# Kernel optimization log

Hardware: AMD Instinct MI355X
Metric: run time of the kernel (lower is better)

## Reference

```python
import jax, jax.numpy as jnp
import numpy as np

NUM_BUCKETS = 32
MAX_DISTANCE = 128
N_HEADS = 16
D_KV = 64


def relative_position_bucket(rel, num_buckets=NUM_BUCKETS, max_distance=MAX_DISTANCE):
    # bidirectional (encoder) bucketing, matches the torch reference
    nb = num_buckets // 2
    ret = (rel > 0).astype(jnp.int32) * nb
    rp = jnp.abs(rel)
    max_exact = nb // 2
    is_small = rp < max_exact
    # guard log(0); masked out by is_small anyway
    large = max_exact + (
        jnp.log(jnp.maximum(rp, 1).astype(jnp.float32) / max_exact)
        / np.log(max_distance / max_exact)
        * (nb - max_exact)
    ).astype(jnp.int32)
    large = jnp.minimum(large, nb - 1)
    return ret + jnp.where(is_small, rp, large)


def compute_bias(rel_bias_table, q_len, k_len):
    q_pos = jnp.arange(q_len)[:, None]
    k_pos = jnp.arange(k_len)[None, :]
    buckets = relative_position_bucket(k_pos - q_pos)  # [S, K]
    bias = rel_bias_table[buckets]                      # [S, K, H]
    return jnp.transpose(bias, (2, 0, 1))[None]         # [1, H, S, K]


def setup_inputs() -> dict:
    key = jax.random.key(0)
    ks = jax.random.split(key, 6)
    d_model, inner = 1024, N_HEADS * D_KV
    scale = 1.0 / np.sqrt(d_model)
    return {
        "hidden_states": jax.random.normal(ks[0], (4, 2048, d_model), jnp.float32),
        "Wq": jax.random.normal(ks[1], (d_model, inner), jnp.float32) * scale,
        "Wk": jax.random.normal(ks[2], (d_model, inner), jnp.float32) * scale,
        "Wv": jax.random.normal(ks[3], (d_model, inner), jnp.float32) * scale,
        "Wo": jax.random.normal(ks[4], (inner, d_model), jnp.float32) * scale,
        "rel_bias_table": jax.random.normal(ks[5], (NUM_BUCKETS, N_HEADS), jnp.float32),
    }


def reference(hidden_states, Wq, Wk, Wv, Wo, rel_bias_table):
    B, S, _ = hidden_states.shape
    K_len = S  # self-attention (key_value_states is None)
    q = (hidden_states @ Wq).reshape(B, S, N_HEADS, D_KV)
    k = (hidden_states @ Wk).reshape(B, K_len, N_HEADS, D_KV)
    v = (hidden_states @ Wv).reshape(B, K_len, N_HEADS, D_KV)
    # NOTE: T5 attention has no 1/sqrt(d_kv) scaling
    scores = jnp.einsum("bshd,bkhd->bhsk", q, k)
    pos_bias = compute_bias(rel_bias_table, S, K_len)
    attn = jax.nn.softmax(scores + pos_bias, axis=-1)
    out = jnp.einsum("bhsk,bkhd->bshd", attn, v).reshape(B, S, N_HEADS * D_KV)
    out = out @ Wo
    return (out, pos_bias)
```

## Files before the change

### kernel.cpp

```cpp
#include <hip/hip_runtime.h>
#include <cstdint>
#include <cstddef>

typedef unsigned short u16;
typedef unsigned int u32;
typedef __attribute__((ext_vector_type(8))) short bf16x8;
typedef __attribute__((ext_vector_type(4))) float f32x4;
typedef __attribute__((ext_vector_type(16))) float f32x16;
typedef __attribute__((ext_vector_type(2))) unsigned int u32x2;

#define MFMA(a, b, c)   __builtin_amdgcn_mfma_f32_16x16x32_bf16((a), (b), (c), 0, 0, 0)
#define MFMA32(a, b, c) __builtin_amdgcn_mfma_f32_32x32x16_bf16((a), (b), (c), 0, 0, 0)

typedef const __attribute__((address_space(1))) void gv1_t;
typedef __attribute__((address_space(3))) void lv3_t;
#define GLOAD_LDS16(g, l) __builtin_amdgcn_global_load_lds((gv1_t*)(g), (lv3_t*)(l), 16, 0, 0)

#define BATCH 4
#define SEQ 2048
#define DMODEL 1024
#define NHEAD 16
#define MROWS (BATCH * SEQ)
#define QKVN (3 * DMODEL)

#define LOG2E 1.44269504088896340736f

__device__ __forceinline__ u16 f2bf(float f) {
  u32 x = __builtin_bit_cast(u32, f);
  x += 0x7fffu + ((x >> 16) & 1u);
  return (u16)(x >> 16);
}

__device__ __forceinline__ u32 pkbf(float a, float b) {
  return (u32)f2bf(a) | ((u32)f2bf(b) << 16);
}

__device__ __forceinline__ u32x2 plswap(u32 a, u32 b) {
  return __builtin_amdgcn_permlane32_swap(a, b, false, false);
}

extern "C" __device__ float __ocml_exp2_f32(float);
__device__ __forceinline__ float exp2fast(float x) {
#if __has_builtin(__builtin_amdgcn_exp2f)
  return __builtin_amdgcn_exp2f(x);
#else
  return __ocml_exp2_f32(x);
#endif
}

__global__ __launch_bounds__(256) void convert_h(const float* __restrict__ H,
                                                 u16* __restrict__ Hb) {
  size_t i = (size_t)blockIdx.x * 1024 + threadIdx.x * 4;
  float4 v = *(const float4*)&H[i];
  uint2 o;
  o.x = pkbf(v.x, v.y);
  o.y = pkbf(v.z, v.w);
  *(uint2*)&Hb[i] = o;
}

__global__ void transpose_w(const float* __restrict__ Wq, const float* __restrict__ Wk,
                            const float* __restrict__ Wv, const float* __restrict__ Wo,
                            u16* __restrict__ Wt) {
  __shared__ u16 Ts[32][33];
  const float* W = (blockIdx.z == 0) ? Wq : (blockIdx.z == 1) ? Wk
                   : (blockIdx.z == 2) ? Wv : Wo;
  const float s = (blockIdx.z == 0) ? LOG2E : 1.0f;
  int x = threadIdx.x, y0 = threadIdx.y;
  int r0 = blockIdx.y * 32, c0 = blockIdx.x * 32;
  for (int yy = y0; yy < 32; yy += 8)
    Ts[yy][x] = f2bf(W[(size_t)(r0 + yy) * 1024 + c0 + x] * s);
  __syncthreads();
  for (int yy = y0; yy < 32; yy += 8)
    Wt[(size_t)(blockIdx.z * 1024 + c0 + yy) * 1024 + r0 + x] = Ts[x][yy];
}

__device__ __forceinline__ int rel_bucket(int rel) {
  int ret = (rel > 0) ? 16 : 0;
  int rp = (rel < 0) ? -rel : rel;
  if (rp < 8) return ret + rp;
  int i = 0;
  i += (rp >= 12); i += (rp >= 16); i += (rp >= 23); i += (rp >= 32);
  i += (rp >= 46); i += (rp >= 64); i += (rp >= 91);
  return ret + 8 + i;
}

__global__ __launch_bounds__(256) void build_bias_rel(const float* __restrict__ tbl,
                                                      float* __restrict__ brel,
                                                      float* __restrict__ brel2) {
  int h = blockIdx.x;
  for (int rix = threadIdx.x; rix < 4095; rix += 256) {
    float v = tbl[rel_bucket(rix - 2047) * NHEAD + h];
    brel[h * 4096 + rix] = v;
    brel2[h * 4096 + rix] = v * LOG2E;
  }
}

__global__ __launch_bounds__(256) void gemm_bf16k(const u16* __restrict__ A,
                                                  const u16* __restrict__ Bt,
                                                  u16* __restrict__ Cb, float* __restrict__ Cf,
                                                  int M, int N, int K) {
  __shared__ u16 As[128 * 32];
  __shared__ u16 Bs[128 * 32];
  const int t = threadIdx.x;
  const int w = t >> 6, lane = t & 63, quad = lane >> 4, l15 = lane & 15;
  const int wr = w >> 1, wc = w & 1;

  const int nwg = gridDim.x * gridDim.y;
  const int orig = blockIdx.y * gridDim.x + blockIdx.x;
  const int wg = (orig & 7) * (nwg >> 3) + (orig >> 3);
  const int bx = wg % gridDim.x, by = wg / gridDim.x;
  const int row0 = by * 128, col0 = bx * 128;

  f32x4 acc[4][4];
  #pragma unroll
  for (int i = 0; i < 4; ++i)
    #pragma unroll
    for (int j = 0; j < 4; ++j) acc[i][j] = (f32x4){0.f, 0.f, 0.f, 0.f};

  const int srow = lane >> 2, scol = (lane & 3) * 8;

  for (int k0 = 0; k0 < K; k0 += 32) {
    #pragma unroll
    for (int p = 0; p < 2; ++p) {
      const int rb = w * 32 + p * 16;
      GLOAD_LDS16(&A[(size_t)(row0 + rb + srow) * K + k0 + scol], &As[rb * 32]);
      GLOAD_LDS16(&Bt[(size_t)(col0 + rb + srow) * K + k0 + scol], &Bs[rb * 32]);
    }
    __syncthreads();
    bf16x8 af[4], bfr[4];
    #pragma unroll
    for (int i = 0; i < 4; ++i)
      af[i] = *(const bf16x8*)&As[(wr * 64 + i * 16 + l15) * 32 + quad * 8];
    #pragma unroll
    for (int j = 0; j < 4; ++j)
      bfr[j] = *(const bf16x8*)&Bs[(wc * 64 + j * 16 + l15) * 32 + quad * 8];
    #pragma unroll
    for (int i = 0; i < 4; ++i)
      #pragma unroll
      for (int j = 0; j < 4; ++j)
        acc[i][j] = MFMA(af[i], bfr[j], acc[i][j]);
    __syncthreads();
  }
  #pragma unroll
  for (int i = 0; i < 4; ++i) {
    #pragma unroll
    for (int j = 0; j < 4; ++j) {
      int col = col0 + wc * 64 + j * 16 + l15;
      #pragma unroll
      for (int r = 0; r < 4; ++r) {
        int row = row0 + wr * 64 + i * 16 + quad * 4 + r;
        if (Cb) Cb[(size_t)row * N + col] = f2bf(acc[i][j][r]);
        else    Cf[(size_t)row * N + col] = acc[i][j][r];
      }
    }
  }
}

__global__ __launch_bounds__(256) void transpose_v(const u16* __restrict__ QKV,
                                                   u16* __restrict__ Vt) {
  __shared__ u16 Ts[64 * 72];
  int st = blockIdx.x, bh = blockIdx.y;
  int b = bh >> 4, h = bh & 15;
  int t = threadIdx.x;
  #pragma unroll
  for (int p = 0; p < 2; ++p) {
    int c = t * 2 + p, r = c >> 3, cc = (c & 7) * 8;
    *(uint4*)&Ts[r * 72 + cc] =
        *(const uint4*)&QKV[(size_t)(b * SEQ + st * 64 + r) * QKVN + 2 * DMODEL + h * 64 + cc];
  }
  __syncthreads();
  #pragma unroll
  for (int p = 0; p < 2; ++p) {
    int c = t * 2 + p, d = c >> 3, s8 = (c & 7) * 8;
    union { u16 u[8]; uint4 v; } tmp;
    #pragma unroll
    for (int jj = 0; jj < 8; ++jj) tmp.u[jj] = Ts[(s8 + jj) * 72 + d];
    *(uint4*)&Vt[((size_t)(bh * 64 + d)) * SEQ + st * 64 + s8] = tmp.v;
  }
}

__global__ __launch_bounds__(256) void attn_fused(const u16* __restrict__ QKV,
                                                  const u16* __restrict__ Vt,
                                                  const float* __restrict__ brel,
                                                  const float* __restrict__ brel2,
                                                  u16* __restrict__ Aout,
                                                  float* __restrict__ pb) {
  __shared__ u16 Ks[2][64 * 72];
  __shared__ u16 Vs[2][64 * 72];
  const int orig = blockIdx.y * gridDim.x + blockIdx.x;
  const int wg = (orig & 7) * 128 + (orig >> 3);
  const int qt = wg & 15, bh = wg >> 4;
  const int b = bh >> 4, h = bh & 15;
  const int t = threadIdx.x;
  const int w = t >> 6, lane = t & 63, l31 = lane & 31, h5 = lane >> 5;
  const int qb = qt * 128;
  const int qw0 = qb + w * 32;
  const int qr = qw0 + l31;

  const float cpos = brel2[h * 4096 + 4040];
  const float cneg = brel2[h * 4096 + 54];
  const float cpu  = brel[h * 4096 + 4040];
  const float cnu  = brel[h * 4096 + 54];

  const u16* qptr = QKV + (size_t)(b * SEQ + qr) * QKVN + h * 64 + h5 * 8;
  bf16x8 qf[4];
  #pragma unroll
  for (int ks = 0; ks < 4; ++ks) qf[ks] = *(const bf16x8*)(qptr + ks * 16);

  float lsum = 0.f;
  f32x16 oacc[2];
  #pragma unroll
  for (int m = 0; m < 2; ++m)
    #pragma unroll
    for (int i = 0; i < 16; ++i) oacc[m][i] = 0.f;

  const int c0 = t * 2, c1 = c0 + 1;
  const int r0s = c0 >> 3, cc0 = (c0 & 7) * 8;
  const int r1s = c1 >> 3, cc1 = (c1 & 7) * 8;
  const size_t krow = (size_t)(b * SEQ) * QKVN + DMODEL + h * 64;
  const size_t vtrow = (size_t)bh * 64;
  const float* brow = brel2 + h * 4096 + 2047;

  uint4 ka0 = *(const uint4*)&QKV[krow + (size_t)r0s * QKVN + cc0];
  uint4 ka1 = *(const uint4*)&QKV[krow + (size_t)r1s * QKVN + cc1];
  uint4 va0 = *(const uint4*)&Vt[(vtrow + r0s) * SEQ + cc0];
  uint4 va1 = *(const uint4*)&Vt[(vtrow + r1s) * SEQ + cc1];
  *(uint4*)&Ks[0][r0s * 72 + cc0] = ka0;
  *(uint4*)&Ks[0][r1s * 72 + cc1] = ka1;
  *(uint4*)&Vs[0][r0s * 72 + cc0] = va0;
  *(uint4*)&Vs[0][r1s * 72 + cc1] = va1;
  __syncthreads();

  #pragma unroll 2
  for (int ti = 0; ti < SEQ / 64; ++ti) {
    const int kb = ti * 64;
    const int cur = ti & 1;
    const u16* Kc = Ks[cur];
    const u16* Vc = Vs[cur];

    if (ti + 1 < SEQ / 64) {
      ka0 = *(const uint4*)&QKV[krow + (size_t)(kb + 64 + r0s) * QKVN + cc0];
      ka1 = *(const uint4*)&QKV[krow + (size_t)(kb + 64 + r1s) * QKVN + cc1];
      va0 = *(const uint4*)&Vt[(vtrow + r0s) * SEQ + kb + 64 + cc0];
      va1 = *(const uint4*)&Vt[(vtrow + r1s) * SEQ + kb + 64 + cc1];
    }

    f32x16 sc[2];
    __builtin_amdgcn_s_setprio(1);
    #pragma unroll
    for (int m = 0; m < 2; ++m) {
      #pragma unroll
      for (int i = 0; i < 16; ++i) sc[m][i] = 0.f;
      #pragma unroll
      for (int ks = 0; ks < 4; ++ks) {
        bf16x8 kf = *(const bf16x8*)&Kc[(m * 32 + l31) * 72 + ks * 16 + h5 * 8];
        sc[m] = MFMA32(kf, qf[ks], sc[m]);
      }
    }
    __builtin_amdgcn_s_setprio(0);

    if ((ti & 3) == b) {
      const int pr = qb + (t >> 1);
      const int pc = kb + (t & 1) * 32;
      float* po = pb + ((size_t)(h * SEQ + pr)) * SEQ + pc;
      const int lo = pc - pr;
      if (lo >= 91 || lo + 31 <= -91) {
        const float c = (lo >= 91) ? cpu : cnu;
        const float4 vv = {c, c, c, c};
        #pragma unroll
        for (int i = 0; i < 8; ++i) *(float4*)&po[i * 4] = vv;
      } else {
        const float* bb = brel + h * 4096 + 2047 - pr + pc;
        #pragma unroll
        for (int i = 0; i < 8; ++i) {
          float4 vv;
          vv.x = bb[i * 4]; vv.y = bb[i * 4 + 1];
          vv.z = bb[i * 4 + 2]; vv.w = bb[i * 4 + 3];
          *(float4*)&po[i * 4] = vv;
        }
      }
    }

    bf16x8 bp[4];
    #pragma unroll
    for (int m = 0; m < 2; ++m) {
      const int kb32 = kb + 32 * m;
      if (kb32 >= qw0 + 122) {
        #pragma unroll
        for (int i = 0; i < 16; ++i) sc[m][i] += cpos;
      } else if (kb32 <= qw0 - 122) {
        #pragma unroll
        for (int i = 0; i < 16; ++i) sc[m][i] += cneg;
      } else {
        const float* bb = brow + kb32 + 4 * h5 - qr;
        #pragma unroll
        for (int i = 0; i < 16; ++i) sc[m][i] += bb[(i & 3) + 8 * (i >> 2)];
      }
      u32 w0[4], w1[4];
      #pragma unroll
      for (int tt = 0; tt < 4; ++tt) {
        float p0 = exp2fast(sc[m][4 * tt + 0]);
        float p1 = exp2fast(sc[m][4 * tt + 1]);
        float p2 = exp2fast(sc[m][4 * tt + 2]);
        float p3 = exp2fast(sc[m][4 * tt + 3]);
        lsum += (p0 + p1) + (p2 + p3);
        w0[tt] = pkbf(p0, p1);
        w1[tt] = pkbf(p2, p3);
      }
      u32x2 r0 = plswap(w0[0], w0[1]);
      u32x2 r1 = plswap(w1[0], w1[1]);
      u32x2 r2 = plswap(w0[2], w0[3]);
      u32x2 r3 = plswap(w1[2], w1[3]);
      union { u32 u[4]; bf16x8 v; } q0, q1;
      q0.u[0] = r0.x; q0.u[1] = r1.x; q0.u[2] = r0.y; q0.u[3] = r1.y;
      q1.u[0] = r2.x; q1.u[1] = r3.x; q1.u[2] = r2.y; q1.u[3] = r3.y;
      bp[2 * m]     = q0.v;
      bp[2 * m + 1] = q1.v;
    }

    __builtin_amdgcn_s_setprio(1);
    #pragma unroll
    for (int m2 = 0; m2 < 2; ++m2)
      #pragma unroll
      for (int ks = 0; ks < 4; ++ks) {
        bf16x8 vf = *(const bf16x8*)&Vc[(m2 * 32 + l31) * 72 + ks * 16 + h5 * 8];
        oacc[m2] = MFMA32(vf, bp[ks], oacc[m2]);
      }
    __builtin_amdgcn_s_setprio(0);

    if (ti + 1 < SEQ / 64) {
      u16* Kn = Ks[cur ^ 1];
      u16* Vn = Vs[cur ^ 1];
      *(uint4*)&Kn[r0s * 72 + cc0] = ka0;
      *(uint4*)&Kn[r1s * 72 + cc1] = ka1;
      *(uint4*)&Vn[r0s * 72 + cc0] = va0;
      *(uint4*)&Vn[r1s * 72 + cc1] = va1;
    }
    __syncthreads();
  }

  lsum += __shfl_xor(lsum, 32);
  const float inv = 1.0f / lsum;
  const size_t rowb = (size_t)(b * SEQ + qr) * DMODEL + h * 64;
  #pragma unroll
  for (int m2 = 0; m2 < 2; ++m2)
    #pragma unroll
    for (int tt = 0; tt < 4; ++tt) {
      uint2 o;
      o.x = pkbf(oacc[m2][4 * tt + 0] * inv, oacc[m2][4 * tt + 1] * inv);
      o.y = pkbf(oacc[m2][4 * tt + 2] * inv, oacc[m2][4 * tt + 3] * inv);
      *(uint2*)&Aout[rowb + 32 * m2 + 8 * tt + 4 * h5] = o;
    }
}

extern "C" void kernel_launch(void* const* d_in, const int* in_sizes, int n_in,
                              void* d_out, int out_size, void* d_ws, size_t ws_size,
                              hipStream_t stream) {
  (void)in_sizes; (void)n_in; (void)out_size; (void)ws_size;
  const float* H   = (const float*)d_in[0];
  const float* Wq  = (const float*)d_in[1];
  const float* Wk  = (const float*)d_in[2];
  const float* Wv  = (const float*)d_in[3];
  const float* Wo  = (const float*)d_in[4];
  const float* tbl = (const float*)d_in[5];

  float* out = (float*)d_out;
  float* pos_bias = out + (size_t)MROWS * DMODEL;

  char* ws = (char*)d_ws;
  u16* Hb     = (u16*)(ws);
  u16* Wt     = (u16*)(ws + 16777216);
  u16* QKV    = (u16*)(ws + 25165824);
  u16* Vt     = (u16*)(ws + 75497472);
  float* brel  = (float*)(ws + 92274688);
  float* brel2 = (float*)(ws + 92536832);

  convert_h<<<8192, 256, 0, stream>>>(H, Hb);
  transpose_w<<<dim3(32, 32, 4), dim3(32, 8), 0, stream>>>(Wq, Wk, Wv, Wo, Wt);
  build_bias_rel<<<16, 256, 0, stream>>>(tbl, brel, brel2);

  gemm_bf16k<<<dim3(QKVN / 128, MROWS / 128), 256, 0, stream>>>(
      Hb, Wt, QKV, nullptr, MROWS, QKVN, DMODEL);
  transpose_v<<<dim3(32, 64), 256, 0, stream>>>(QKV, Vt);
  attn_fused<<<dim3(16, 64), 256, 0, stream>>>(QKV, Vt, brel, brel2,
                                               Hb , pos_bias);
  gemm_bf16k<<<dim3(DMODEL / 128, MROWS / 128), 256, 0, stream>>>(
      Hb, Wt + (size_t)QKVN * DMODEL, nullptr, out, MROWS, DMODEL, DMODEL);
}
```

Before: 571.8 us.

## Fuse V transpose into QKV GEMM epilogue and software-pipeline PV MFMA

```diff
diff --git a/kernel.cpp b/kernel.cpp
--- a/kernel.cpp
+++ b/kernel.cpp
@@ -98,6 +98,7 @@
 __global__ __launch_bounds__(256) void gemm_bf16k(const u16* __restrict__ A,
                                                   const u16* __restrict__ Bt,
                                                   u16* __restrict__ Cb, float* __restrict__ Cf,
+                                                  u16* __restrict__ Vt,
                                                   int M, int N, int K) {
   __shared__ u16 As[128 * 32];
   __shared__ u16 Bs[128 * 32];
@@ -145,37 +146,25 @@
   for (int i = 0; i < 4; ++i) {
     #pragma unroll
     for (int j = 0; j < 4; ++j) {
-      int col = col0 + wc * 64 + j * 16 + l15;
-      #pragma unroll
-      for (int r = 0; r < 4; ++r) {
-        int row = row0 + wr * 64 + i * 16 + quad * 4 + r;
-        if (Cb) Cb[(size_t)row * N + col] = f2bf(acc[i][j][r]);
-        else    Cf[(size_t)row * N + col] = acc[i][j][r];
-      }
-    }
-  }
-}
-
-__global__ __launch_bounds__(256) void transpose_v(const u16* __restrict__ QKV,
-                                                   u16* __restrict__ Vt) {
-  __shared__ u16 Ts[64 * 72];
-  int st = blockIdx.x, bh = blockIdx.y;
-  int b = bh >> 4, h = bh & 15;
-  int t = threadIdx.x;
-  #pragma unroll
-  for (int p = 0; p < 2; ++p) {
-    int c = t * 2 + p, r = c >> 3, cc = (c & 7) * 8;
-    *(uint4*)&Ts[r * 72 + cc] =
-        *(const uint4*)&QKV[(size_t)(b * SEQ + st * 64 + r) * QKVN + 2 * DMODEL + h * 64 + cc];
-  }
-  __syncthreads();
-  #pragma unroll
-  for (int p = 0; p < 2; ++p) {
-    int c = t * 2 + p, d = c >> 3, s8 = (c & 7) * 8;
-    union { u16 u[8]; uint4 v; } tmp;
-    #pragma unroll
-    for (int jj = 0; jj < 8; ++jj) tmp.u[jj] = Ts[(s8 + jj) * 72 + d];
-    *(uint4*)&Vt[((size_t)(bh * 64 + d)) * SEQ + st * 64 + s8] = tmp.v;
+      const int col = col0 + wc * 64 + j * 16 + l15;
+      const int srow0 = row0 + wr * 64 + i * 16 + quad * 4;
+      if (Cf) {
+        #pragma unroll
+        for (int r = 0; r < 4; ++r)
+          Cf[(size_t)(srow0 + r) * N + col] = acc[i][j][r];
+      } else if (!Vt || col < 2 * DMODEL) {
+        #pragma unroll
+        for (int r = 0; r < 4; ++r)
+          Cb[(size_t)(srow0 + r) * N + col] = f2bf(acc[i][j][r]);
+      } else {
+        const int c2 = col - 2 * DMODEL, hh = c2 >> 6, dd = c2 & 63;
+        const int bb = srow0 >> 11, ss = srow0 & (SEQ - 1);
+        uint2 o;
+        o.x = pkbf(acc[i][j][0], acc[i][j][1]);
+        o.y = pkbf(acc[i][j][2], acc[i][j][3]);
+        *(uint2*)&Vt[((size_t)(bb * 16 + hh) * 64 + dd) * SEQ + ss] = o;
+      }
+    }
   }
 }
 
@@ -231,6 +220,9 @@
   *(uint4*)&Vs[0][r1s * 72 + cc1] = va1;
   __syncthreads();
 
+  bf16x8 vreg[8];
+  bf16x8 bpp[4];
+
   #pragma unroll 2
   for (int ti = 0; ti < SEQ / 64; ++ti) {
     const int kb = ti * 64;
@@ -245,8 +237,15 @@
       va1 = *(const uint4*)&Vt[(vtrow + r1s) * SEQ + kb + 64 + cc1];
     }
 
+    __builtin_amdgcn_s_setprio(1);
+    if (ti > 0) {
+      #pragma unroll
+      for (int m2 = 0; m2 < 2; ++m2)
+        #pragma unroll
+        for (int ks = 0; ks < 4; ++ks)
+          oacc[m2] = MFMA32(vreg[m2 * 4 + ks], bpp[ks], oacc[m2]);
+    }
     f32x16 sc[2];
-    __builtin_amdgcn_s_setprio(1);
     #pragma unroll
     for (int m = 0; m < 2; ++m) {
       #pragma unroll
@@ -281,7 +280,6 @@
       }
     }
 
-    bf16x8 bp[4];
     #pragma unroll
     for (int m = 0; m < 2; ++m) {
       const int kb32 = kb + 32 * m;
@@ -314,19 +312,15 @@
       union { u32 u[4]; bf16x8 v; } q0, q1;
       q0.u[0] = r0.x; q0.u[1] = r1.x; q0.u[2] = r0.y; q0.u[3] = r1.y;
       q1.u[0] = r2.x; q1.u[1] = r3.x; q1.u[2] = r2.y; q1.u[3] = r3.y;
-      bp[2 * m]     = q0.v;
-      bp[2 * m + 1] = q1.v;
-    }
-
-    __builtin_amdgcn_s_setprio(1);
+      bpp[2 * m]     = q0.v;
+      bpp[2 * m + 1] = q1.v;
+    }
+
     #pragma unroll
     for (int m2 = 0; m2 < 2; ++m2)
       #pragma unroll
-      for (int ks = 0; ks < 4; ++ks) {
-        bf16x8 vf = *(const bf16x8*)&Vc[(m2 * 32 + l31) * 72 + ks * 16 + h5 * 8];
-        oacc[m2] = MFMA32(vf, bp[ks], oacc[m2]);
-      }
-    __builtin_amdgcn_s_setprio(0);
+      for (int ks = 0; ks < 4; ++ks)
+        vreg[m2 * 4 + ks] = *(const bf16x8*)&Vc[(m2 * 32 + l31) * 72 + ks * 16 + h5 * 8];
 
     if (ti + 1 < SEQ / 64) {
       u16* Kn = Ks[cur ^ 1];
@@ -338,6 +332,14 @@
     }
     __syncthreads();
   }
+
+  __builtin_amdgcn_s_setprio(1);
+  #pragma unroll
+  for (int m2 = 0; m2 < 2; ++m2)
+    #pragma unroll
+    for (int ks = 0; ks < 4; ++ks)
+      oacc[m2] = MFMA32(vreg[m2 * 4 + ks], bpp[ks], oacc[m2]);
+  __builtin_amdgcn_s_setprio(0);
 
   lsum += __shfl_xor(lsum, 32);
   const float inv = 1.0f / lsum;
@@ -380,10 +382,9 @@
   build_bias_rel<<<16, 256, 0, stream>>>(tbl, brel, brel2);
 
   gemm_bf16k<<<dim3(QKVN / 128, MROWS / 128), 256, 0, stream>>>(
-      Hb, Wt, QKV, nullptr, MROWS, QKVN, DMODEL);
-  transpose_v<<<dim3(32, 64), 256, 0, stream>>>(QKV, Vt);
+      Hb, Wt, QKV, nullptr, Vt, MROWS, QKVN, DMODEL);
   attn_fused<<<dim3(16, 64), 256, 0, stream>>>(QKV, Vt, brel, brel2,
                                                Hb , pos_bias);
   gemm_bf16k<<<dim3(DMODEL / 128, MROWS / 128), 256, 0, stream>>>(
-      Hb, Wt + (size_t)QKVN * DMODEL, nullptr, out, MROWS, DMODEL, DMODEL);
-}
+      Hb, Wt + (size_t)QKVN * DMODEL, nullptr, out, nullptr, MROWS, DMODEL, DMODEL);
+}
```

Result: no change. 566.4 us (-1.0%).
